# Optimization experiments

Hardware: AMD Instinct MI355X
Metric: run time of the kernel (lower is better)

The kernel has to match this reference:

```python
import jax, jax.numpy as jnp
import numpy as np

TAU = 0.2
EPS = 1e-12  # matches torch F.normalize eps


def setup_inputs() -> dict:
    key = jax.random.key(0)
    k1, k2 = jax.random.split(key)
    N, D = 8192, 128
    h1 = jax.random.normal(k1, (N, D), dtype=jnp.float32)
    h2 = jax.random.normal(k2, (N, D), dtype=jnp.float32)
    return {"h1": h1, "h2": h2}


def _l2norm(x):
    # torch.nn.functional.normalize: x / max(||x||, eps)
    n = jnp.sqrt(jnp.sum(x * x, axis=1, keepdims=True))
    return x / jnp.maximum(n, EPS)


def _nt_xent(h1, h2):
    h1n = _l2norm(h1)
    h2n = _l2norm(h2)
    inter = jnp.exp((h1n @ h1n.T) / TAU)  # [N, N]
    intra = jnp.exp((h1n @ h2n.T) / TAU)  # [N, N]
    pos = jnp.diagonal(intra)
    neg = inter.sum(axis=1) + intra.sum(axis=1) - jnp.diagonal(inter)
    return -jnp.log(pos / neg)  # [N]


def reference(h1, h2):
    l1 = _nt_xent(h1, h2)
    l2 = _nt_xent(h2, h1)
    return jnp.mean((l1 + l2) * 0.5)
```

## Files before the change

kernel.cpp:

```cpp
#include <hip/hip_runtime.h>
#include <math.h>


constexpr int D = 128;
constexpr float E5 = 148.4131591025766f;

typedef __attribute__((ext_vector_type(16))) float f32x16;

__global__ __launch_bounds__(256) void normalize_kernel(
    const float2* __restrict__ h1, const float2* __restrict__ h2,
    unsigned short* __restrict__ Gx, float* __restrict__ d12,
    float* __restrict__ rsum, float* __restrict__ out, int N)
{
    const float SC = sqrtf(5.0f * 1.44269504088896340736f);
    int gid = blockIdx.x * 256 + threadIdx.x;
    if (gid < 2 * N) rsum[gid] = 0.f;
    if (gid == 0) out[0] = 0.f;

    int row  = blockIdx.x * 4 + (threadIdx.x >> 6);
    int lane = threadIdx.x & 63;
    float2 u = h1[(size_t)row * 64 + lane];
    float2 w = h2[(size_t)row * 64 + lane];
    float ss1 = u.x * u.x + u.y * u.y;
    float ss2 = w.x * w.x + w.y * w.y;
    float s12 = u.x * w.x + u.y * w.y;
#pragma unroll
    for (int off = 32; off > 0; off >>= 1) {
        ss1 += __shfl_xor(ss1, off, 64);
        ss2 += __shfl_xor(ss2, off, 64);
        s12 += __shfl_xor(s12, off, 64);
    }
    float n1 = fmaxf(sqrtf(ss1), 1e-12f);
    float n2 = fmaxf(sqrtf(ss2), 1e-12f);
    float c1 = SC / n1, c2 = SC / n2;
    int p1 = __builtin_amdgcn_cvt_pk_fp8_f32(u.x * c1, u.y * c1, 0, false);
    int p2 = __builtin_amdgcn_cvt_pk_fp8_f32(w.x * c2, w.y * c2, 0, false);
    Gx[(size_t)row * 64 + lane]           = (unsigned short)(p1 & 0xffff);
    Gx[(size_t)(N + row) * 64 + lane]     = (unsigned short)(p2 & 0xffff);
    if (lane == 0) d12[row] = 5.f * s12 / (n1 * n2);
}

__global__ __launch_bounds__(256, 2) void gram_mfma_kernel(
    const unsigned char* __restrict__ G, float* __restrict__ rsum, int N)
{
    const int I = blockIdx.x;
    int nT = 4, dBase = 0;
    if (blockIdx.y < 16) { dBase = blockIdx.y * 4; }
    else if (I < 64)     { nT = 1; dBase = 64; }
    else return;

    __shared__ long Ys[2][2048];

    const int tx   = threadIdx.x;
    const int lane = tx & 63;
    const int l32  = lane & 31, lhi = lane >> 5;
    const int wi   = (tx >> 6) >> 1, wj = (tx >> 6) & 1;
    const int iBase = I * 128;

    auto jStrip = [&](int t) { return (I + dBase + t) & 127; };

    long a[2][8];
#pragma unroll
    for (int st = 0; st < 2; ++st) {
        const unsigned char* xp =
            G + (size_t)(iBase + wi * 64 + st * 32 + l32) * D + lhi * 8;
#pragma unroll
        for (int ks = 0; ks < 8; ++ks)
            a[st][ks] = *(const long*)(xp + ks * 16);
    }

    float racc0[16], racc1[16];
#pragma unroll
    for (int r = 0; r < 16; ++r) { racc0[r] = 0.f; racc1[r] = 0.f; }
    float cpA[4] = {0.f, 0.f, 0.f, 0.f};
    float cpB[4] = {0.f, 0.f, 0.f, 0.f};

    long2 v[4];
    {
        const long2* yp = (const long2*)(G + (size_t)jStrip(0) * 128 * D);
#pragma unroll
        for (int i = 0; i < 4; ++i) v[i] = yp[i * 256 + tx];
    }

    const int j0 = wj * 64 + l32;
    const int j1 = j0 + 32;
    const int sw = l32 & 15;

    for (int t = 0; t < nT; ++t) {
        long* buf = Ys[t & 1];
#pragma unroll
        for (int i = 0; i < 4; ++i) {
            int chunk = i * 256 + tx;
            int j = chunk >> 3, c = chunk & 7;
            int base = ((2 * c) ^ (j & 15)) & ~1;
            long2 w = v[i];
            if (j & 1) { long tmp = w.x; w.x = w.y; w.y = tmp; }
            *(long2*)&buf[j * 16 + base] = w;
        }
        __syncthreads();

        if (t + 1 < nT) {
            const long2* yp =
                (const long2*)(G + (size_t)jStrip(t + 1) * 128 * D);
#pragma unroll
            for (int i = 0; i < 4; ++i) v[i] = yp[i * 256 + tx];
        }

        f32x16 acc00, acc01, acc10, acc11;
#pragma unroll
        for (int r = 0; r < 16; ++r) {
            acc00[r] = 0.f; acc01[r] = 0.f; acc10[r] = 0.f; acc11[r] = 0.f;
        }

#pragma unroll
        for (int ks = 0; ks < 8; ++ks) {
            int f = 2 * ks + lhi;
            long b0 = buf[j0 * 16 + (f ^ sw)];
            long b1 = buf[j1 * 16 + (f ^ sw)];
            acc00 = __builtin_amdgcn_mfma_f32_32x32x16_fp8_fp8(a[0][ks], b0, acc00, 0, 0, 0);
            acc10 = __builtin_amdgcn_mfma_f32_32x32x16_fp8_fp8(a[1][ks], b0, acc10, 0, 0, 0);
            acc01 = __builtin_amdgcn_mfma_f32_32x32x16_fp8_fp8(a[0][ks], b1, acc01, 0, 0, 0);
            acc11 = __builtin_amdgcn_mfma_f32_32x32x16_fp8_fp8(a[1][ks], b1, acc11, 0, 0, 0);
        }

        float c0 = 0.f, c1 = 0.f;
#pragma unroll
        for (int r = 0; r < 16; ++r) {
            float e00 = __builtin_amdgcn_exp2f(acc00[r]);
            float e01 = __builtin_amdgcn_exp2f(acc01[r]);
            float e10 = __builtin_amdgcn_exp2f(acc10[r]);
            float e11 = __builtin_amdgcn_exp2f(acc11[r]);
            racc0[r] += e00 + e01;
            racc1[r] += e10 + e11;
            c0 += e00 + e10;
            c1 += e01 + e11;
        }
        if ((dBase + t) != 0) { cpA[t] = c0; cpB[t] = c1; }
    }

#pragma unroll
    for (int r = 0; r < 16; ++r) {
        float s0 = racc0[r], s1 = racc1[r];
#pragma unroll
        for (int off = 1; off < 32; off <<= 1) {
            s0 += __shfl_xor(s0, off, 64);
            s1 += __shfl_xor(s1, off, 64);
        }
        if (l32 == 0) {
            int rowm = (r & 3) + 8 * (r >> 2) + 4 * lhi;
            atomicAdd(&rsum[iBase + wi * 64 + rowm], s0);
            atomicAdd(&rsum[iBase + wi * 64 + 32 + rowm], s1);
        }
    }

#pragma unroll
    for (int t = 0; t < 4; ++t) {
        if (t >= nT) break;
        if ((dBase + t) == 0) continue;
        float c0 = cpA[t], c1 = cpB[t];
        c0 += __shfl_xor(c0, 32, 64);
        c1 += __shfl_xor(c1, 32, 64);
        if (lane < 32) {
            int jb = jStrip(t) * 128;
            atomicAdd(&rsum[jb + j0], c0);
            atomicAdd(&rsum[jb + j1], c1);
        }
    }
}

__global__ __launch_bounds__(256) void loss_reduce_kernel(
    const float* __restrict__ rsum, const float* __restrict__ d12,
    float* __restrict__ out, int N)
{
    __shared__ float sm[256];
    float s = 0.f;
    for (int i = blockIdx.x * 256 + threadIdx.x; i < N; i += gridDim.x * 256) {
        float neg1 = rsum[i] - E5;
        float neg2 = rsum[N + i] - E5;
        s += 0.5f * (logf(neg1) + logf(neg2)) - d12[i];
    }
    sm[threadIdx.x] = s;
    __syncthreads();
    for (int w = 128; w > 0; w >>= 1) {
        if (threadIdx.x < w) sm[threadIdx.x] += sm[threadIdx.x + w];
        __syncthreads();
    }
    if (threadIdx.x == 0) atomicAdd(out, sm[0] / (float)N);
}

extern "C" void kernel_launch(void* const* d_in, const int* in_sizes, int n_in,
                              void* d_out, int out_size, void* d_ws, size_t ws_size,
                              hipStream_t stream) {
    const float* h1 = (const float*)d_in[0];
    const float* h2 = (const float*)d_in[1];
    const int N = in_sizes[0] / D;

    unsigned char* G = (unsigned char*)d_ws;
    float* rsum = (float*)(G + (size_t)2 * N * D);
    float* d12  = rsum + 2 * N;
    float* out  = (float*)d_out;

    normalize_kernel<<<N / 4, 256, 0, stream>>>(
        (const float2*)h1, (const float2*)h2,
        (unsigned short*)G, d12, rsum, out, N);

    dim3 grid(128, 17, 1);
    gram_mfma_kernel<<<grid, 256, 0, stream>>>(G, rsum, N);

    loss_reduce_kernel<<<32, 256, 0, stream>>>(rsum, d12, out, N);
}
```

Measured before the change: 117.5 us.

## Prepack fp8 operands in MFMA fragment order and load B directly from global

The normalize kernel now writes the fp8 normalized vectors in a fragment-major layout matching the 32x32x16 MFMA operand order. The gram kernel drops its shared-memory staging, swizzle, __syncthreads and register double-buffering, and loads each wave's B fragments straight from global/L2 as coalesced 8-byte reads. This removes LDS traffic and block-level barriers. In exchange each wave fetches its B data independently, so global/L2 load traffic rises, and the loads are no longer prefetched one tile ahead to overlap with compute.

```diff
diff --git a/kernel.cpp b/kernel.cpp
--- a/kernel.cpp
+++ b/kernel.cpp
@@ -9,7 +9,7 @@
 
 __global__ __launch_bounds__(256) void normalize_kernel(
     const float2* __restrict__ h1, const float2* __restrict__ h2,
-    unsigned short* __restrict__ Gx, float* __restrict__ d12,
+    unsigned short* __restrict__ P16, float* __restrict__ d12,
     float* __restrict__ rsum, float* __restrict__ out, int N)
 {
     const float SC = sqrtf(5.0f * 1.44269504088896340736f);
@@ -35,13 +35,17 @@
     float c1 = SC / n1, c2 = SC / n2;
     int p1 = __builtin_amdgcn_cvt_pk_fp8_f32(u.x * c1, u.y * c1, 0, false);
     int p2 = __builtin_amdgcn_cvt_pk_fp8_f32(w.x * c2, w.y * c2, 0, false);
-    Gx[(size_t)row * 64 + lane]           = (unsigned short)(p1 & 0xffff);
-    Gx[(size_t)(N + row) * 64 + lane]     = (unsigned short)(p2 & 0xffff);
+    int r1 = row, r2 = N + row;
+    int fi = lane >> 2, li = lane & 3;
+    P16[(size_t)(((r1 >> 5) * 16 + fi) * 128) + (r1 & 31) * 4 + li] =
+        (unsigned short)(p1 & 0xffff);
+    P16[(size_t)(((r2 >> 5) * 16 + fi) * 128) + (r2 & 31) * 4 + li] =
+        (unsigned short)(p2 & 0xffff);
     if (lane == 0) d12[row] = 5.f * s12 / (n1 * n2);
 }
 
 __global__ __launch_bounds__(256, 2) void gram_mfma_kernel(
-    const unsigned char* __restrict__ G, float* __restrict__ rsum, int N)
+    const unsigned char* __restrict__ P, float* __restrict__ rsum, int N)
 {
     const int I = blockIdx.x;
     int nT = 4, dBase = 0;
@@ -49,24 +53,20 @@
     else if (I < 64)     { nT = 1; dBase = 64; }
     else return;
 
-    __shared__ long Ys[2][2048];
-
     const int tx   = threadIdx.x;
     const int lane = tx & 63;
     const int l32  = lane & 31, lhi = lane >> 5;
     const int wi   = (tx >> 6) >> 1, wj = (tx >> 6) & 1;
     const int iBase = I * 128;
 
-    auto jStrip = [&](int t) { return (I + dBase + t) & 127; };
-
     long a[2][8];
 #pragma unroll
     for (int st = 0; st < 2; ++st) {
         const unsigned char* xp =
-            G + (size_t)(iBase + wi * 64 + st * 32 + l32) * D + lhi * 8;
+            P + (size_t)((I * 4 + wi * 2 + st) * 16 + lhi) * 256 + l32 * 8;
 #pragma unroll
         for (int ks = 0; ks < 8; ++ks)
-            a[st][ks] = *(const long*)(xp + ks * 16);
+            a[st][ks] = *(const long*)(xp + ks * 512);
     }
 
     float racc0[16], racc1[16];
@@ -75,35 +75,19 @@
     float cpA[4] = {0.f, 0.f, 0.f, 0.f};
     float cpB[4] = {0.f, 0.f, 0.f, 0.f};
 
-    long2 v[4];
-    {
-        const long2* yp = (const long2*)(G + (size_t)jStrip(0) * 128 * D);
-#pragma unroll
-        for (int i = 0; i < 4; ++i) v[i] = yp[i * 256 + tx];
-    }
-
     const int j0 = wj * 64 + l32;
     const int j1 = j0 + 32;
-    const int sw = l32 & 15;
 
     for (int t = 0; t < nT; ++t) {
-        long* buf = Ys[t & 1];
+        const int J = (I + dBase + t) & 127;
+        const unsigned char* pb =
+            P + (size_t)((J * 4 + wj * 2) * 16 + lhi) * 256 + l32 * 8;
+
+        long b0[8], b1[8];
 #pragma unroll
-        for (int i = 0; i < 4; ++i) {
-            int chunk = i * 256 + tx;
-            int j = chunk >> 3, c = chunk & 7;
-            int base = ((2 * c) ^ (j & 15)) & ~1;
-            long2 w = v[i];
-            if (j & 1) { long tmp = w.x; w.x = w.y; w.y = tmp; }
-            *(long2*)&buf[j * 16 + base] = w;
-        }
-        __syncthreads();
-
-        if (t + 1 < nT) {
-            const long2* yp =
-                (const long2*)(G + (size_t)jStrip(t + 1) * 128 * D);
-#pragma unroll
-            for (int i = 0; i < 4; ++i) v[i] = yp[i * 256 + tx];
+        for (int ks = 0; ks < 8; ++ks) {
+            b0[ks] = *(const long*)(pb + ks * 512);
+            b1[ks] = *(const long*)(pb + 4096 + ks * 512);
         }
 
         f32x16 acc00, acc01, acc10, acc11;
@@ -114,13 +98,10 @@
 
 #pragma unroll
         for (int ks = 0; ks < 8; ++ks) {
-            int f = 2 * ks + lhi;
-            long b0 = buf[j0 * 16 + (f ^ sw)];
-            long b1 = buf[j1 * 16 + (f ^ sw)];
-            acc00 = __builtin_amdgcn_mfma_f32_32x32x16_fp8_fp8(a[0][ks], b0, acc00, 0, 0, 0);
-            acc10 = __builtin_amdgcn_mfma_f32_32x32x16_fp8_fp8(a[1][ks], b0, acc10, 0, 0, 0);
-            acc01 = __builtin_amdgcn_mfma_f32_32x32x16_fp8_fp8(a[0][ks], b1, acc01, 0, 0, 0);
-            acc11 = __builtin_amdgcn_mfma_f32_32x32x16_fp8_fp8(a[1][ks], b1, acc11, 0, 0, 0);
+            acc00 = __builtin_amdgcn_mfma_f32_32x32x16_fp8_fp8(a[0][ks], b0[ks], acc00, 0, 0, 0);
+            acc10 = __builtin_amdgcn_mfma_f32_32x32x16_fp8_fp8(a[1][ks], b0[ks], acc10, 0, 0, 0);
+            acc01 = __builtin_amdgcn_mfma_f32_32x32x16_fp8_fp8(a[0][ks], b1[ks], acc01, 0, 0, 0);
+            acc11 = __builtin_amdgcn_mfma_f32_32x32x16_fp8_fp8(a[1][ks], b1[ks], acc11, 0, 0, 0);
         }
 
         float c0 = 0.f, c1 = 0.f;
@@ -161,7 +142,7 @@
         c0 += __shfl_xor(c0, 32, 64);
         c1 += __shfl_xor(c1, 32, 64);
         if (lane < 32) {
-            int jb = jStrip(t) * 128;
+            int jb = ((I + dBase + t) & 127) * 128;
             atomicAdd(&rsum[jb + j0], c0);
             atomicAdd(&rsum[jb + j1], c1);
         }
@@ -195,17 +176,17 @@
     const float* h2 = (const float*)d_in[1];
     const int N = in_sizes[0] / D;
 
-    unsigned char* G = (unsigned char*)d_ws;
-    float* rsum = (float*)(G + (size_t)2 * N * D);
+    unsigned char* P = (unsigned char*)d_ws;
+    float* rsum = (float*)(P + (size_t)2 * N * D);
     float* d12  = rsum + 2 * N;
     float* out  = (float*)d_out;
 
     normalize_kernel<<<N / 4, 256, 0, stream>>>(
         (const float2*)h1, (const float2*)h2,
-        (unsigned short*)G, d12, rsum, out, N);
+        (unsigned short*)P, d12, rsum, out, N);
 
     dim3 grid(128, 17, 1);
-    gram_mfma_kernel<<<grid, 256, 0, stream>>>(G, rsum, N);
+    gram_mfma_kernel<<<grid, 256, 0, stream>>>(P, rsum, N);
 
     loss_reduce_kernel<<<32, 256, 0, stream>>>(rsum, d12, out, N);
 }
```

Result: faster. 107.9 us (-8.2%).
